# Optimization experiments

Hardware: AMD Instinct MI355X
Metric: run time of the kernel (lower is better)

## Reference

```python
import jax, jax.numpy as jnp
import numpy as np

N_PROT = 20000   # protein table rows
D = 256          # hidden_dim
T = 262144       # total (drug, pathway, protein) memberships
G = 16384        # number of (drug, pathway) groups
N_DRUGS = 4096


def setup_inputs() -> dict:
    key = jax.random.key(0)
    k1, k2, k3, k4, k5, k6 = jax.random.split(key, 6)
    protein_h = jax.random.normal(k1, (N_PROT, D), dtype=jnp.float32)
    member_protein_idx = jax.random.randint(k2, (T,), 0, N_PROT)
    member_seg = jnp.sort(jax.random.randint(k3, (T,), 0, G))
    group_to_drug = jnp.sort(jax.random.randint(k4, (G,), 0, N_DRUGS))
    attn_w = jax.random.normal(k5, (D,), dtype=jnp.float32) / np.sqrt(D)
    proj_W = jax.random.normal(k6, (D, D), dtype=jnp.float32) / np.sqrt(D)
    proj_b = jnp.zeros((D,), dtype=jnp.float32)
    return dict(protein_h=protein_h, member_protein_idx=member_protein_idx,
                member_seg=member_seg, group_to_drug=group_to_drug,
                attn_w=attn_w, proj_W=proj_W, proj_b=proj_b)


def reference(protein_h, member_protein_idx, member_seg, group_to_drug,
              attn_w, proj_W, proj_b):
    # Gather protein embeddings for all (drug, pathway) memberships.  [T, D]
    ph = protein_h[member_protein_idx]
    # Attention logits (Linear(D, 1, bias=False)).  [T]
    s = ph @ attn_w
    # Segment softmax within each pathway group (stable).
    smax = jax.ops.segment_max(s, member_seg, num_segments=G)
    smax = jax.lax.stop_gradient(jnp.where(jnp.isfinite(smax), smax, 0.0))
    e = jnp.exp(s - smax[member_seg])
    denom = jax.ops.segment_sum(e, member_seg, num_segments=G)
    w = e / denom[member_seg]                                    # [T]
    # Attention-weighted pool per pathway group.  [G, D]
    pooled = jax.ops.segment_sum(w[:, None] * ph, member_seg, num_segments=G)
    # Mean over non-empty pathway groups per drug.
    cnt = jax.ops.segment_sum(jnp.ones_like(s), member_seg, num_segments=G)
    nonempty = (cnt > 0).astype(protein_h.dtype)                 # [G]
    drug_sum = jax.ops.segment_sum(pooled, group_to_drug, num_segments=N_DRUGS)
    drug_cnt = jax.ops.segment_sum(nonempty, group_to_drug, num_segments=N_DRUGS)
    out = drug_sum / jnp.maximum(drug_cnt, 1.0)[:, None]          # [N_DRUGS, D]
    # Dropout is identity at eval time; final projection + ReLU.
    return jax.nn.relu(out @ proj_W.T + proj_b)
```

## Files before the change

### kernel.cpp

```cpp
#include <hip/hip_runtime.h>
#include <math.h>

#define HD 256

typedef unsigned int uint32;
typedef __attribute__((ext_vector_type(8))) short bf16x8;
typedef __attribute__((ext_vector_type(4))) float f32x4;

__device__ inline unsigned short f2bf(float f) {
  uint32 u = __float_as_uint(f);
  return (unsigned short)((u + 0x7fffu + ((u >> 16) & 1u)) >> 16);
}
__device__ inline float bflo(uint32 v) { return __uint_as_float(v << 16); }
__device__ inline float bfhi(uint32 v) { return __uint_as_float(v & 0xffff0000u); }

__global__ __launch_bounds__(256) void prep_kernel(
    const int* __restrict__ mseg, int T, int G, int* __restrict__ gstart,
    const int* __restrict__ g2d, int ND, int* __restrict__ dstart,
    const float* __restrict__ W, int NW, unsigned short* __restrict__ Wbf,
    const float* __restrict__ protein_h, const float* __restrict__ attn_w,
    int np, float* __restrict__ etbl, unsigned short* __restrict__ wph,
    int nbb) {
  int b = blockIdx.x;
  if (b < nbb) {
    int t = b * 256 + threadIdx.x;
    if (t <= T) {
      int cur  = (t < T) ? mseg[t] : G;
      int prev = (t == 0) ? -1 : mseg[t - 1];
      for (int g = prev + 1; g <= cur; ++g) gstart[g] = t;
    }
    if (t <= G) {
      int cur  = (t < G) ? g2d[t] : ND;
      int prev = (t == 0) ? -1 : g2d[t - 1];
      for (int d = prev + 1; d <= cur; ++d) dstart[d] = t;
    }
    if (t < NW) Wbf[t] = f2bf(W[t]);
    return;
  }
  int wave = threadIdx.x >> 6, lane = threadIdx.x & 63;
  int p = (b - nbb) * 4 + wave;
  if (p >= np) return;
  float4 w = ((const float4*)attn_w)[lane];
  float4 v = ((const float4*)(protein_h + (size_t)p * HD))[lane];
  float s = v.x * w.x + v.y * w.y + v.z * w.z + v.w * w.w;
#pragma unroll
  for (int o = 32; o > 0; o >>= 1) s += __shfl_xor(s, o, 64);
  float e = __expf(s);
  if (lane == 0) etbl[p] = e;
  ushort4 st;
  st.x = f2bf(e * v.x); st.y = f2bf(e * v.y);
  st.z = f2bf(e * v.z); st.w = f2bf(e * v.w);
  *(ushort4*)(wph + ((size_t)(lane >> 4) * np + p) * 64 + (lane & 15) * 4) = st;
}

__global__ __launch_bounds__(256) void coef_kernel(
    const int* __restrict__ midx, const float* __restrict__ etbl,
    const int* __restrict__ gstart, int G, uint2* __restrict__ cw) {
  int q = blockIdx.x * 16 + (threadIdx.x >> 4);
  int ql = threadIdx.x & 15;
  if (q >= G) return;
  int beg = gstart[q], end = gstart[q + 1];
  if (beg >= end) return;
  float d = 0.f;
  for (int c = beg + ql; c < end; c += 16) d += etbl[midx[c]];
  d += __shfl_xor(d, 1, 64); d += __shfl_xor(d, 2, 64);
  d += __shfl_xor(d, 4, 64); d += __shfl_xor(d, 8, 64);
  float inv = 1.f / d;
  for (int c = beg + ql; c < end; c += 16) {
    cw[c] = make_uint2((uint32)midx[c], __float_as_uint(inv));
  }
}

__global__ __launch_bounds__(64) void drug_pool_kernel(
    const unsigned short* __restrict__ wph, const uint2* __restrict__ cw,
    const int* __restrict__ gstart, const int* __restrict__ dstart,
    int ND, int np, unsigned short* __restrict__ dmean) {
  int lane = threadIdx.x;
  int B = blockIdx.x;
  int xcd = B & 7;
  int chunk = xcd >> 1;
  int d0 = ((B >> 3) * 2 + (xcd & 1)) * 2;
  if (d0 >= ND) return;
  const unsigned short* slice = wph + (size_t)chunk * np * 64;
  int quarter = lane >> 4, qlane = lane & 15;
  for (int di = 0; di < 2; ++di) {
    int d = d0 + di;
    if (d >= ND) break;
    int gb = dstart[d], ge = dstart[d + 1];
    int mbeg = gstart[gb], mend = gstart[ge];
    int cnt = 0;
    for (int base = gb; base < ge; base += 64) {
      int gg = base + lane;
      bool ne = (gg < ge) && (gstart[gg + 1] > gstart[gg]);
      cnt += (int)__popcll(__ballot(ne));
    }
    float4 acc = make_float4(0.f, 0.f, 0.f, 0.f);
    for (int c = mbeg; c < mend; c += 64) {
      int cn = mend - c; if (cn > 64) cn = 64;
#pragma unroll 4
      for (int t = 0; t < cn; t += 4) {
        int src = t + quarter;
        if (src < cn) {
          uint2 cwv = cw[c + src];
          float cf = __uint_as_float(cwv.y);
          uint2 v = *(const uint2*)(slice + ((size_t)cwv.x << 6) + (qlane << 2));
          acc.x += cf * bflo(v.x); acc.y += cf * bfhi(v.x);
          acc.z += cf * bflo(v.y); acc.w += cf * bfhi(v.y);
        }
      }
    }
    acc.x += __shfl_xor(acc.x, 16, 64); acc.x += __shfl_xor(acc.x, 32, 64);
    acc.y += __shfl_xor(acc.y, 16, 64); acc.y += __shfl_xor(acc.y, 32, 64);
    acc.z += __shfl_xor(acc.z, 16, 64); acc.z += __shfl_xor(acc.z, 32, 64);
    acc.w += __shfl_xor(acc.w, 16, 64); acc.w += __shfl_xor(acc.w, 32, 64);
    float inv = 1.f / fmaxf((float)cnt, 1.f);
    if (quarter == 0) {
      ushort4 st;
      st.x = f2bf(acc.x * inv); st.y = f2bf(acc.y * inv);
      st.z = f2bf(acc.z * inv); st.w = f2bf(acc.w * inv);
      *(ushort4*)(dmean + (size_t)d * HD + (chunk << 6) + (qlane << 2)) = st;
    }
  }
}

#define GM 16
__global__ __launch_bounds__(512) void gemm_kernel(
    const unsigned short* __restrict__ A, const unsigned short* __restrict__ Wbf,
    const float* __restrict__ bias, float* __restrict__ out) {
  int wave = threadIdx.x >> 6, lane = threadIdx.x & 63;
  int m0 = blockIdx.x * GM;
  int n0 = wave * 32;
  int arow = lane & 15;
  int apack = lane >> 4;
  f32x4 acc[2] = {};
#pragma unroll
  for (int k0 = 0; k0 < HD; k0 += 32) {
    int k = k0 + apack * 8;
    bf16x8 af = *(const bf16x8*)(A + (size_t)(m0 + arow) * HD + k);
#pragma unroll
    for (int t = 0; t < 2; ++t) {
      int col = n0 + t * 16 + arow;
      bf16x8 bfr = *(const bf16x8*)(Wbf + (size_t)col * HD + k);
      acc[t] = __builtin_amdgcn_mfma_f32_16x16x32_bf16(af, bfr, acc[t], 0, 0, 0);
    }
  }
  int rbase = m0 + (lane >> 4) * 4;
#pragma unroll
  for (int t = 0; t < 2; ++t) {
    int col = n0 + t * 16 + (lane & 15);
    float bv = bias[col];
#pragma unroll
    for (int j = 0; j < 4; ++j) {
      out[(size_t)(rbase + j) * HD + col] = fmaxf(acc[t][j] + bv, 0.f);
    }
  }
}

extern "C" void kernel_launch(void* const* d_in, const int* in_sizes, int n_in,
                              void* d_out, int out_size, void* d_ws, size_t ws_size,
                              hipStream_t stream) {
  const float* protein_h = (const float*)d_in[0];
  const int*   midx      = (const int*)d_in[1];
  const int*   mseg      = (const int*)d_in[2];
  const int*   g2d       = (const int*)d_in[3];
  const float* attn_w    = (const float*)d_in[4];
  const float* proj_W    = (const float*)d_in[5];
  const float* proj_b    = (const float*)d_in[6];
  float* out = (float*)d_out;

  const int NPROT = in_sizes[0] / HD;
  const int T  = in_sizes[1];
  const int G  = in_sizes[3];
  const int NW = in_sizes[5];
  const int ND = out_size / HD;

  char* ws = (char*)d_ws;
  int* gstart = (int*)ws;
  int* dstart = gstart + (G + 1);
  size_t off = (((size_t)(G + 1) + (size_t)(ND + 1)) * sizeof(int) + 255) & ~(size_t)255;
  float* etbl = (float*)(ws + off);
  off += (((size_t)NPROT * sizeof(float)) + 255) & ~(size_t)255;
  unsigned short* Wbf = (unsigned short*)(ws + off);
  off += (((size_t)NW * sizeof(unsigned short)) + 255) & ~(size_t)255;
  unsigned short* wph = (unsigned short*)(ws + off);
  off += (((size_t)NPROT * HD * sizeof(unsigned short)) + 255) & ~(size_t)255;
  uint2* cw = (uint2*)(ws + off);
  off += (((size_t)T * sizeof(uint2)) + 255) & ~(size_t)255;
  unsigned short* dmean = (unsigned short*)(ws + off);

  int nmax = (T > G ? T : G) + 1;
  int nbb = (nmax + 255) / 256;
  int npb = (NPROT + 3) / 4;
  prep_kernel<<<nbb + npb, 256, 0, stream>>>(
      mseg, T, G, gstart, g2d, ND, dstart, proj_W, NW, Wbf,
      protein_h, attn_w, NPROT, etbl, wph, nbb);
  coef_kernel<<<(G + 15) / 16, 256, 0, stream>>>(midx, etbl, gstart, G, cw);
  drug_pool_kernel<<<8 * ((ND + 3) / 4), 64, 0, stream>>>(
      wph, cw, gstart, dstart, ND, NPROT, dmean);
  gemm_kernel<<<ND / GM, 512, 0, stream>>>(dmean, Wbf, proj_b, out);
}
```

Measured before the change: 60.45 us.

## Fuse softmax denominator computation into drug pooling kernel, drop coef pass

Removes the separate coef_kernel that computed per-group softmax denominators and wrote a (row, inv) array for every membership. The drug pooling kernel now walks each drug's groups itself, loads member indices once per 64-chunk and broadcasts them via shuffles, sums etbl for the denominator, accumulates unscaled rows, and scales by the inverse per group. It also handles one drug per block instead of two, doubling the grid. This saves a kernel launch and the T-sized intermediate write/read, but adds a per-group serial loop with a wave reduction for each group, which is costly for small groups.

```diff
diff --git a/kernel.cpp b/kernel.cpp
--- a/kernel.cpp
+++ b/kernel.cpp
@@ -53,73 +53,62 @@
   *(ushort4*)(wph + ((size_t)(lane >> 4) * np + p) * 64 + (lane & 15) * 4) = st;
 }
 
-__global__ __launch_bounds__(256) void coef_kernel(
-    const int* __restrict__ midx, const float* __restrict__ etbl,
-    const int* __restrict__ gstart, int G, uint2* __restrict__ cw) {
-  int q = blockIdx.x * 16 + (threadIdx.x >> 4);
-  int ql = threadIdx.x & 15;
-  if (q >= G) return;
-  int beg = gstart[q], end = gstart[q + 1];
-  if (beg >= end) return;
-  float d = 0.f;
-  for (int c = beg + ql; c < end; c += 16) d += etbl[midx[c]];
-  d += __shfl_xor(d, 1, 64); d += __shfl_xor(d, 2, 64);
-  d += __shfl_xor(d, 4, 64); d += __shfl_xor(d, 8, 64);
-  float inv = 1.f / d;
-  for (int c = beg + ql; c < end; c += 16) {
-    cw[c] = make_uint2((uint32)midx[c], __float_as_uint(inv));
-  }
-}
-
 __global__ __launch_bounds__(64) void drug_pool_kernel(
-    const unsigned short* __restrict__ wph, const uint2* __restrict__ cw,
-    const int* __restrict__ gstart, const int* __restrict__ dstart,
-    int ND, int np, unsigned short* __restrict__ dmean) {
+    const unsigned short* __restrict__ wph, const int* __restrict__ midx,
+    const float* __restrict__ etbl, const int* __restrict__ gstart,
+    const int* __restrict__ dstart, int ND, int np,
+    unsigned short* __restrict__ dmean) {
   int lane = threadIdx.x;
   int B = blockIdx.x;
   int xcd = B & 7;
   int chunk = xcd >> 1;
-  int d0 = ((B >> 3) * 2 + (xcd & 1)) * 2;
-  if (d0 >= ND) return;
+  int d = (B >> 3) * 2 + (xcd & 1);
+  if (d >= ND) return;
   const unsigned short* slice = wph + (size_t)chunk * np * 64;
   int quarter = lane >> 4, qlane = lane & 15;
-  for (int di = 0; di < 2; ++di) {
-    int d = d0 + di;
-    if (d >= ND) break;
-    int gb = dstart[d], ge = dstart[d + 1];
-    int mbeg = gstart[gb], mend = gstart[ge];
-    int cnt = 0;
-    for (int base = gb; base < ge; base += 64) {
-      int gg = base + lane;
-      bool ne = (gg < ge) && (gstart[gg + 1] > gstart[gg]);
-      cnt += (int)__popcll(__ballot(ne));
-    }
-    float4 acc = make_float4(0.f, 0.f, 0.f, 0.f);
-    for (int c = mbeg; c < mend; c += 64) {
-      int cn = mend - c; if (cn > 64) cn = 64;
+  int gb = dstart[d], ge = dstart[d + 1];
+  float4 acc = make_float4(0.f, 0.f, 0.f, 0.f);
+  float cnt = 0.f;
+  int mb = gstart[gb];
+  for (int g = gb; g < ge; ++g) {
+    int me = gstart[g + 1];
+    if (me > mb) {
+      float4 gacc = make_float4(0.f, 0.f, 0.f, 0.f);
+      float den = 0.f;
+      for (int c = mb; c < me; c += 64) {
+        int cn = me - c; if (cn > 64) cn = 64;
+        int myrow = midx[c + (lane < cn ? lane : 0)];
+        if (lane < cn) den += etbl[myrow];
 #pragma unroll 4
-      for (int t = 0; t < cn; t += 4) {
-        int src = t + quarter;
-        if (src < cn) {
-          uint2 cwv = cw[c + src];
-          float cf = __uint_as_float(cwv.y);
-          uint2 v = *(const uint2*)(slice + ((size_t)cwv.x << 6) + (qlane << 2));
-          acc.x += cf * bflo(v.x); acc.y += cf * bfhi(v.x);
-          acc.z += cf * bflo(v.y); acc.w += cf * bfhi(v.y);
+        for (int t = 0; t < cn; t += 4) {
+          int src = t + quarter;
+          int row = __shfl(myrow, src, 64);
+          if (src < cn) {
+            uint2 v = *(const uint2*)(slice + ((size_t)row << 6) + (qlane << 2));
+            gacc.x += bflo(v.x); gacc.y += bfhi(v.x);
+            gacc.z += bflo(v.y); gacc.w += bfhi(v.y);
+          }
         }
       }
+#pragma unroll
+      for (int o = 32; o > 0; o >>= 1) den += __shfl_xor(den, o, 64);
+      float inv = 1.f / den;
+      acc.x += gacc.x * inv; acc.y += gacc.y * inv;
+      acc.z += gacc.z * inv; acc.w += gacc.w * inv;
+      cnt += 1.f;
     }
-    acc.x += __shfl_xor(acc.x, 16, 64); acc.x += __shfl_xor(acc.x, 32, 64);
-    acc.y += __shfl_xor(acc.y, 16, 64); acc.y += __shfl_xor(acc.y, 32, 64);
-    acc.z += __shfl_xor(acc.z, 16, 64); acc.z += __shfl_xor(acc.z, 32, 64);
-    acc.w += __shfl_xor(acc.w, 16, 64); acc.w += __shfl_xor(acc.w, 32, 64);
-    float inv = 1.f / fmaxf((float)cnt, 1.f);
-    if (quarter == 0) {
-      ushort4 st;
-      st.x = f2bf(acc.x * inv); st.y = f2bf(acc.y * inv);
-      st.z = f2bf(acc.z * inv); st.w = f2bf(acc.w * inv);
-      *(ushort4*)(dmean + (size_t)d * HD + (chunk << 6) + (qlane << 2)) = st;
-    }
+    mb = me;
+  }
+  acc.x += __shfl_xor(acc.x, 16, 64); acc.x += __shfl_xor(acc.x, 32, 64);
+  acc.y += __shfl_xor(acc.y, 16, 64); acc.y += __shfl_xor(acc.y, 32, 64);
+  acc.z += __shfl_xor(acc.z, 16, 64); acc.z += __shfl_xor(acc.z, 32, 64);
+  acc.w += __shfl_xor(acc.w, 16, 64); acc.w += __shfl_xor(acc.w, 32, 64);
+  float minv = 1.f / fmaxf(cnt, 1.f);
+  if (quarter == 0) {
+    ushort4 st;
+    st.x = f2bf(acc.x * minv); st.y = f2bf(acc.y * minv);
+    st.z = f2bf(acc.z * minv); st.w = f2bf(acc.w * minv);
+    *(ushort4*)(dmean + (size_t)d * HD + (chunk << 6) + (qlane << 2)) = st;
   }
 }
 
@@ -184,8 +173,6 @@
   off += (((size_t)NW * sizeof(unsigned short)) + 255) & ~(size_t)255;
   unsigned short* wph = (unsigned short*)(ws + off);
   off += (((size_t)NPROT * HD * sizeof(unsigned short)) + 255) & ~(size_t)255;
-  uint2* cw = (uint2*)(ws + off);
-  off += (((size_t)T * sizeof(uint2)) + 255) & ~(size_t)255;
   unsigned short* dmean = (unsigned short*)(ws + off);
 
   int nmax = (T > G ? T : G) + 1;
@@ -194,8 +181,7 @@
   prep_kernel<<<nbb + npb, 256, 0, stream>>>(
       mseg, T, G, gstart, g2d, ND, dstart, proj_W, NW, Wbf,
       protein_h, attn_w, NPROT, etbl, wph, nbb);
-  coef_kernel<<<(G + 15) / 16, 256, 0, stream>>>(midx, etbl, gstart, G, cw);
-  drug_pool_kernel<<<8 * ((ND + 3) / 4), 64, 0, stream>>>(
-      wph, cw, gstart, dstart, ND, NPROT, dmean);
+  drug_pool_kernel<<<8 * ((ND + 1) / 2), 64, 0, stream>>>(
+      wph, midx, etbl, gstart, dstart, ND, NPROT, dmean);
   gemm_kernel<<<ND / GM, 512, 0, stream>>>(dmean, Wbf, proj_b, out);
 }
```

Result: faster. 55.55 us (-8.1%).
